# Performance work log

Hardware: AMD Instinct MI355X
Metric: run time of the kernel (lower is better)

The kernel has to match this reference:

```python
import jax, jax.numpy as jnp
import numpy as np

EMBED_DIM = 1024
NUM_HEADS = 16
NUM_KV_HEADS = 4
HEAD_DIM = 64
GQA_RATIO = NUM_HEADS // NUM_KV_HEADS
SCALE = 1.0 / np.sqrt(HEAD_DIM).astype(np.float32)
B, L = 1, 4096
NUM_SEQS = 8  # 8 packed sequences of length 512


def setup_inputs() -> dict:
    key = jax.random.key(0)
    k1, k2, k3, k4, k5 = jax.random.split(key, 5)
    hidden_states = jax.random.normal(k1, (B, L, EMBED_DIM), dtype=jnp.float32)
    cu_seqlens = (jnp.arange(NUM_SEQS + 1, dtype=jnp.int32) * (L // NUM_SEQS))
    s = 1.0 / np.sqrt(EMBED_DIM)
    Wq = jax.random.normal(k2, (EMBED_DIM, NUM_HEADS * HEAD_DIM), dtype=jnp.float32) * s
    Wk = jax.random.normal(k3, (EMBED_DIM, NUM_KV_HEADS * HEAD_DIM), dtype=jnp.float32) * s
    Wv = jax.random.normal(k4, (EMBED_DIM, NUM_KV_HEADS * HEAD_DIM), dtype=jnp.float32) * s
    Wo = jax.random.normal(k5, (NUM_HEADS * HEAD_DIM, EMBED_DIM), dtype=jnp.float32) * s
    return {"hidden_states": hidden_states, "Wq": Wq, "Wk": Wk, "Wv": Wv, "Wo": Wo,
            "cu_seqlens": cu_seqlens}


def reference(hidden_states, Wq, Wk, Wv, Wo, cu_seqlens):
    b, l, d = hidden_states.shape
    # QKV projections (Linear, no bias)
    q = (hidden_states @ Wq).reshape(b, l, NUM_HEADS, HEAD_DIM)
    k = (hidden_states @ Wk).reshape(b, l, NUM_KV_HEADS, HEAD_DIM)
    v = (hidden_states @ Wv).reshape(b, l, NUM_KV_HEADS, HEAD_DIM)
    # GQA: expand kv heads to num_heads (faithful to module's manual expand)
    k = jnp.repeat(k, GQA_RATIO, axis=2)  # [b, l, H, hd]
    v = jnp.repeat(v, GQA_RATIO, axis=2)
    # [b, H, l, hd]
    q = q.transpose(0, 2, 1, 3)
    k = k.transpose(0, 2, 1, 3)
    v = v.transpose(0, 2, 1, 3)
    # block-diagonal varlen mask from cu_seqlens
    pos = jnp.arange(l, dtype=jnp.int32)
    seq_ids = jnp.searchsorted(cu_seqlens, pos, side='right') - 1  # [l]
    mask = seq_ids[:, None] == seq_ids[None, :]                    # [l, l]
    # dense SDPA with mask
    scores = jnp.einsum('bhqd,bhkd->bhqk', q, k) * SCALE
    scores = jnp.where(mask[None, None], scores, jnp.finfo(scores.dtype).min)
    attn = jax.nn.softmax(scores, axis=-1)
    out = jnp.einsum('bhqk,bhkd->bhqd', attn, v)
    out = out.transpose(0, 2, 1, 3).reshape(b, l, NUM_HEADS * HEAD_DIM)
    return out @ Wo
```

## Files before the change

### kernel.cpp

```cpp
#include <hip/hip_runtime.h>
#include <hip/hip_bf16.h>
#include <stdint.h>
#include <stddef.h>

typedef __attribute__((ext_vector_type(8))) short short8;
typedef __attribute__((ext_vector_type(4))) short short4v;
typedef __attribute__((ext_vector_type(4))) float f32x4;

__device__ inline void store_c(float* p, float v) { *p = v; }
__device__ inline void store_c(__hip_bfloat16* p, float v) { *p = __float2bfloat16(v); }

__device__ __forceinline__ void gld_lds16(const __hip_bfloat16* g, __hip_bfloat16* l)
{
#if __has_builtin(__builtin_amdgcn_global_load_lds)
    __builtin_amdgcn_global_load_lds(
        (const __attribute__((address_space(1))) unsigned int*)g,
        (__attribute__((address_space(3))) unsigned int*)l,
        16, 0, 0);
#else
    *(short8*)((char*)l + (threadIdx.x & 63) * 16) = *(const short8*)g;
#endif
}

__global__ __launch_bounds__(256) void convert_kernel(const float* __restrict__ in,
                                                      __hip_bfloat16* __restrict__ out,
                                                      int n4)
{
    int i = blockIdx.x * blockDim.x + threadIdx.x;
    if (i >= n4) return;
    const f32x4 v = *(const f32x4*)(in + (size_t)i * 4);
    union { __hip_bfloat16 t[4]; short4v s4; } u;
    #pragma unroll
    for (int j = 0; j < 4; ++j) u.t[j] = __float2bfloat16(v[j]);
    *(short4v*)(out + (size_t)i * 4) = u.s4;
}

__global__ __launch_bounds__(256) void transpose_kernel(const float* __restrict__ Wq,
                                                        const float* __restrict__ Wk,
                                                        const float* __restrict__ Wv,
                                                        const float* __restrict__ Wo,
                                                        __hip_bfloat16* __restrict__ Wt)
{
    __shared__ float tile[32][33];
    const int bk = blockIdx.x;
    const int bn = blockIdx.y;
    const int tx = threadIdx.x & 31;
    const int ty = threadIdx.x >> 5;
    const int n0 = bn * 32;

    const float* src; int ld; int col0;
    if (n0 < 1024)      { src = Wq; ld = 1024; col0 = n0; }
    else if (n0 < 1280) { src = Wk; ld = 256;  col0 = n0 - 1024; }
    else if (n0 < 1536) { src = Wv; ld = 256;  col0 = n0 - 1280; }
    else                { src = Wo; ld = 1024; col0 = n0 - 1536; }

    #pragma unroll
    for (int r = 0; r < 4; ++r) {
        int k = ty + 8 * r;
        tile[k][tx] = src[(size_t)(bk * 32 + k) * ld + col0 + tx];
    }
    __syncthreads();
    #pragma unroll
    for (int r = 0; r < 4; ++r) {
        int nl = ty + 8 * r;
        Wt[(size_t)(n0 + nl) * 1024 + bk * 32 + tx] = __float2bfloat16(tile[tx][nl]);
    }
}

__global__ __launch_bounds__(256) void vt_kernel(const __hip_bfloat16* __restrict__ QKV,
                                                 __hip_bfloat16* __restrict__ Vt)
{
    __shared__ __hip_bfloat16 tile[32][34];
    const int j0 = blockIdx.x * 32;
    const int c0 = blockIdx.y * 32;
    const int tx = threadIdx.x & 31;
    const int ty = threadIdx.x >> 5;

    #pragma unroll
    for (int r = 0; r < 4; ++r) {
        int jl = ty + 8 * r;
        int j = j0 + jl;
        int srcrow = (j & ~63) + (j & 3) * 16 + ((j >> 2) & 15);
        tile[jl][tx] = QKV[(size_t)srcrow * 1536 + 1280 + c0 + tx];
    }
    __syncthreads();
    #pragma unroll
    for (int r = 0; r < 4; ++r) {
        int cl = ty + 8 * r;
        Vt[(size_t)(c0 + cl) * 4096 + j0 + tx] = tile[tx][cl];
    }
}

#define BK 32

template <int BM, int BN, typename CT>
__global__ __launch_bounds__(256) void gemm_gld_kernel(const __hip_bfloat16* __restrict__ A,
                                                       const __hip_bfloat16* __restrict__ Bt,
                                                       CT* __restrict__ C,
                                                       int M, int N, int K)
{
    constexpr int MF = BM / 32;
    constexpr int NF = BN / 32;
    __shared__ __align__(16) __hip_bfloat16 As[BM * BK];
    __shared__ __align__(16) __hip_bfloat16 Bs[BN * BK];

    const int tid  = threadIdx.x;
    const int lane = tid & 63;
    const int wave = tid >> 6;
    const int wm = wave >> 1;
    const int wn = wave & 1;
    const int fr = lane & 15;
    const int fk = (lane >> 4) * 8;

    const __hip_bfloat16* Ab = A  + (size_t)(blockIdx.x * BM) * K;
    const __hip_bfloat16* Bb = Bt + (size_t)(blockIdx.y * BN) * K;

    const int srow = lane >> 2;
    const int scol = (lane & 3) * 8;

    f32x4 acc[MF][NF];
    const f32x4 z4 = {0.f, 0.f, 0.f, 0.f};
    #pragma unroll
    for (int i = 0; i < MF; ++i)
        #pragma unroll
        for (int j = 0; j < NF; ++j) acc[i][j] = z4;

    for (int k0 = 0; k0 < K; k0 += BK) {
        for (int i = wave; i < BM / 16; i += 4)
            gld_lds16(Ab + (size_t)(i * 16 + srow) * K + k0 + scol, &As[i * 512]);
        for (int i = wave; i < BN / 16; i += 4)
            gld_lds16(Bb + (size_t)(i * 16 + srow) * K + k0 + scol, &Bs[i * 512]);
        __syncthreads();

        short8 af[MF], bfv[NF];
        #pragma unroll
        for (int mf = 0; mf < MF; ++mf)
            af[mf] = *(const short8*)&As[(wm * (BM / 2) + mf * 16 + fr) * BK + fk];
        #pragma unroll
        for (int nf = 0; nf < NF; ++nf)
            bfv[nf] = *(const short8*)&Bs[(wn * (BN / 2) + nf * 16 + fr) * BK + fk];
        #pragma unroll
        for (int mf = 0; mf < MF; ++mf)
            #pragma unroll
            for (int nf = 0; nf < NF; ++nf)
                acc[mf][nf] = __builtin_amdgcn_mfma_f32_16x16x32_bf16(af[mf], bfv[nf], acc[mf][nf], 0, 0, 0);
        __syncthreads();
    }

    const int crow = blockIdx.x * BM + wm * (BM / 2);
    const int ccol = blockIdx.y * BN + wn * (BN / 2);
    #pragma unroll
    for (int mf = 0; mf < MF; ++mf)
        #pragma unroll
        for (int nf = 0; nf < NF; ++nf)
            #pragma unroll
            for (int r = 0; r < 4; ++r) {
                int row = crow + mf * 16 + (lane >> 4) * 4 + r;
                int col = ccol + nf * 16 + fr;
                store_c(&C[(size_t)row * N + col], acc[mf][nf][r]);
            }
}

__global__ __launch_bounds__(256) void attn_kernel(const __hip_bfloat16* __restrict__ QKV,
                                                   const __hip_bfloat16* __restrict__ Vt,
                                                   __hip_bfloat16* __restrict__ O)
{
    __shared__ __align__(16) __hip_bfloat16 Ks[64 * 64];
    __shared__ __align__(16) __hip_bfloat16 Vts[64 * 64];
    __shared__ __align__(16) __hip_bfloat16 Ps[4][16][72];

    const int tid  = threadIdx.x;
    const int lane = tid & 63;
    const int wave = tid >> 6;
    const int qt = blockIdx.x;
    const int h  = blockIdx.y;
    const int sq = blockIdx.z;
    const int kvh = h >> 2;

    const int fr = lane & 15;
    const int fg = lane >> 4;
    const int fk = fg * 8;

    const int sr = lane >> 3;
    const int scol = ((lane & 7) ^ sr) * 8;

    const int q0 = sq * 512 + qt * 64 + wave * 16;

    short8 qf[2];
    #pragma unroll
    for (int kc = 0; kc < 2; ++kc)
        qf[kc] = *(const short8*)(QKV + (size_t)(q0 + fr) * 1536 + h * 64 + kc * 32 + fk);

    const f32x4 z4 = {0.f, 0.f, 0.f, 0.f};
    f32x4 acc_o[4];
    #pragma unroll
    for (int b = 0; b < 4; ++b) acc_o[b] = z4;

    float m_run[4], l_run[4];
    #pragma unroll
    for (int r = 0; r < 4; ++r) { m_run[r] = -1e30f; l_run[r] = 0.f; }

    const float cs = 0.125f * 1.44269504088896340736f;

    for (int t = 0; t < 8; ++t) {
        const int kvbase = sq * 512 + t * 64;

        #pragma unroll
        for (int i = wave; i < 8; i += 4) {
            gld_lds16(QKV + (size_t)(kvbase + i * 8 + sr) * 1536 + 1024 + kvh * 64 + scol,
                      &Ks[i * 512]);
            gld_lds16(Vt + (size_t)(kvh * 64 + i * 8 + sr) * 4096 + kvbase + scol,
                      &Vts[i * 512]);
        }
        __syncthreads();

        f32x4 s[4];
        #pragma unroll
        for (int b = 0; b < 4; ++b) s[b] = z4;
        #pragma unroll
        for (int kc = 0; kc < 2; ++kc) {
            #pragma unroll
            for (int nf = 0; nf < 4; ++nf) {
                short8 kf = *(const short8*)&Ks[(nf * 16 + fr) * 64 + (((kc * 4 + fg) ^ (fr & 7)) * 8)];
                s[nf] = __builtin_amdgcn_mfma_f32_16x16x32_bf16(qf[kc], kf, s[nf], 0, 0, 0);
            }
        }

        #pragma unroll
        for (int r = 0; r < 4; ++r) {
            float mx = fmaxf(fmaxf(s[0][r], s[1][r]), fmaxf(s[2][r], s[3][r]));
            #pragma unroll
            for (int off = 1; off < 16; off <<= 1)
                mx = fmaxf(mx, __shfl_xor(mx, off));
            float mnew = fmaxf(m_run[r], mx);
            float f = exp2f((m_run[r] - mnew) * cs);
            m_run[r] = mnew;
            float p0 = exp2f((s[0][r] - mnew) * cs);
            float p1 = exp2f((s[1][r] - mnew) * cs);
            float p2 = exp2f((s[2][r] - mnew) * cs);
            float p3 = exp2f((s[3][r] - mnew) * cs);
            l_run[r] = l_run[r] * f + (p0 + p1 + p2 + p3);
            #pragma unroll
            for (int nf = 0; nf < 4; ++nf)
                acc_o[nf][r] *= f;
            int rl = fg * 4 + r;
            union { __hip_bfloat16 h[4]; short4v s4; } pw;
            pw.h[0] = __float2bfloat16(p0);
            pw.h[1] = __float2bfloat16(p1);
            pw.h[2] = __float2bfloat16(p2);
            pw.h[3] = __float2bfloat16(p3);
            *(short4v*)&Ps[wave][rl][fr * 4] = pw.s4;
        }

        #pragma unroll
        for (int kc = 0; kc < 2; ++kc) {
            short8 pa = *(const short8*)&Ps[wave][fr][kc * 32 + fk];
            #pragma unroll
            for (int nf = 0; nf < 4; ++nf) {
                short8 vf = *(const short8*)&Vts[(nf * 16 + fr) * 64 + (((kc * 4 + fg) ^ (fr & 7)) * 8)];
                acc_o[nf] = __builtin_amdgcn_mfma_f32_16x16x32_bf16(pa, vf, acc_o[nf], 0, 0, 0);
            }
        }
        __syncthreads();
    }

    #pragma unroll
    for (int r = 0; r < 4; ++r) {
        float lsum = l_run[r];
        #pragma unroll
        for (int off = 1; off < 16; off <<= 1)
            lsum += __shfl_xor(lsum, off);
        float inv_l = 1.0f / lsum;
        int row = q0 + fg * 4 + r;
        #pragma unroll
        for (int nf = 0; nf < 4; ++nf)
            O[(size_t)row * 1024 + h * 64 + nf * 16 + fr] =
                __float2bfloat16(acc_o[nf][r] * inv_l);
    }
}

extern "C" void kernel_launch(void* const* d_in, const int* in_sizes, int n_in,
                              void* d_out, int out_size, void* d_ws, size_t ws_size,
                              hipStream_t stream)
{
    const float* hs = (const float*)d_in[0];
    const float* Wq = (const float*)d_in[1];
    const float* Wk = (const float*)d_in[2];
    const float* Wv = (const float*)d_in[3];
    const float* Wo = (const float*)d_in[4];

    char* ws = (char*)d_ws;
    __hip_bfloat16* hsb  = (__hip_bfloat16*)(ws);
    __hip_bfloat16* Wt   = (__hip_bfloat16*)(ws + 8388608);
    __hip_bfloat16* QKV  = (__hip_bfloat16*)(ws + 13631488);
    __hip_bfloat16* AOut = (__hip_bfloat16*)(ws + 26214400);
    __hip_bfloat16* Vt   = (__hip_bfloat16*)(ws + 34603008);
    float* out = (float*)d_out;

    convert_kernel<<<4096, 256, 0, stream>>>(hs, hsb, 1048576);
    transpose_kernel<<<dim3(32, 80), 256, 0, stream>>>(Wq, Wk, Wv, Wo, Wt);
    gemm_gld_kernel<64, 128, __hip_bfloat16><<<dim3(64, 12), 256, 0, stream>>>(hsb, Wt, QKV, 4096, 1536, 1024);
    vt_kernel<<<dim3(128, 8), 256, 0, stream>>>(QKV, Vt);
    attn_kernel<<<dim3(8, 16, 8), 256, 0, stream>>>(QKV, Vt, AOut);
    gemm_gld_kernel<64, 128, float><<<dim3(64, 8), 256, 0, stream>>>(AOut, Wt + (size_t)1536 * 1024, out, 4096, 1024, 1024);
}
```

Baseline: 158.9 us.

## Use 128x128 GEMM tiles with BK=64, 8 waves and XOR-swizzled LDS

Replaces the 64x128/BK=32 GEMM with a 128x128 tile kernel using 512 threads, a K step of 64, and an XOR swizzle on the LDS layout so fragment reads avoid bank conflicts. Larger tiles raise reuse per loaded byte and halve the number of barrier-separated K iterations. In exchange the grid shrinks to 384 and 256 blocks, which may underfill the 256 CUs and leave little latency hiding, since there is still no double buffering.

```diff
diff --git a/kernel.cpp b/kernel.cpp
--- a/kernel.cpp
+++ b/kernel.cpp
@@ -91,71 +91,82 @@
     }
 }
 
-#define BK 32
-
-template <int BM, int BN, typename CT>
-__global__ __launch_bounds__(256) void gemm_gld_kernel(const __hip_bfloat16* __restrict__ A,
-                                                       const __hip_bfloat16* __restrict__ Bt,
-                                                       CT* __restrict__ C,
-                                                       int M, int N, int K)
-{
-    constexpr int MF = BM / 32;
-    constexpr int NF = BN / 32;
-    __shared__ __align__(16) __hip_bfloat16 As[BM * BK];
-    __shared__ __align__(16) __hip_bfloat16 Bs[BN * BK];
+template <typename CT>
+__global__ __launch_bounds__(512) void gemm128_kernel(const __hip_bfloat16* __restrict__ A,
+                                                      const __hip_bfloat16* __restrict__ Bt,
+                                                      CT* __restrict__ C,
+                                                      int M, int N, int K)
+{
+    __shared__ __align__(16) __hip_bfloat16 As[128 * 64];
+    __shared__ __align__(16) __hip_bfloat16 Bs[128 * 64];
 
     const int tid  = threadIdx.x;
     const int lane = tid & 63;
     const int wave = tid >> 6;
-    const int wm = wave >> 1;
-    const int wn = wave & 1;
+    const int wr = wave >> 2;
+    const int wc = wave & 3;
     const int fr = lane & 15;
-    const int fk = (lane >> 4) * 8;
-
-    const __hip_bfloat16* Ab = A  + (size_t)(blockIdx.x * BM) * K;
-    const __hip_bfloat16* Bb = Bt + (size_t)(blockIdx.y * BN) * K;
-
-    const int srow = lane >> 2;
-    const int scol = (lane & 3) * 8;
-
-    f32x4 acc[MF][NF];
+    const int fg = lane >> 4;
+
+    const __hip_bfloat16* Ab = A  + (size_t)(blockIdx.x * 128) * K;
+    const __hip_bfloat16* Bb = Bt + (size_t)(blockIdx.y * 128) * K;
+
+    const int srow8 = lane >> 3;
+    const int sslot = (lane & 7) ^ srow8;
+
+    f32x4 acc[4][2];
     const f32x4 z4 = {0.f, 0.f, 0.f, 0.f};
     #pragma unroll
-    for (int i = 0; i < MF; ++i)
-        #pragma unroll
-        for (int j = 0; j < NF; ++j) acc[i][j] = z4;
-
-    for (int k0 = 0; k0 < K; k0 += BK) {
-        for (int i = wave; i < BM / 16; i += 4)
-            gld_lds16(Ab + (size_t)(i * 16 + srow) * K + k0 + scol, &As[i * 512]);
-        for (int i = wave; i < BN / 16; i += 4)
-            gld_lds16(Bb + (size_t)(i * 16 + srow) * K + k0 + scol, &Bs[i * 512]);
+    for (int i = 0; i < 4; ++i)
+        #pragma unroll
+        for (int j = 0; j < 2; ++j) acc[i][j] = z4;
+
+    for (int k0 = 0; k0 < K; k0 += 64) {
+        #pragma unroll
+        for (int i = 0; i < 2; ++i) {
+            int c = wave * 2 + i;
+            gld_lds16(Ab + (size_t)(c * 8 + srow8) * K + k0 + sslot * 8, &As[c * 512]);
+        }
+        #pragma unroll
+        for (int i = 0; i < 2; ++i) {
+            int c = wave * 2 + i;
+            gld_lds16(Bb + (size_t)(c * 8 + srow8) * K + k0 + sslot * 8, &Bs[c * 512]);
+        }
         __syncthreads();
 
-        short8 af[MF], bfv[NF];
-        #pragma unroll
-        for (int mf = 0; mf < MF; ++mf)
-            af[mf] = *(const short8*)&As[(wm * (BM / 2) + mf * 16 + fr) * BK + fk];
-        #pragma unroll
-        for (int nf = 0; nf < NF; ++nf)
-            bfv[nf] = *(const short8*)&Bs[(wn * (BN / 2) + nf * 16 + fr) * BK + fk];
-        #pragma unroll
-        for (int mf = 0; mf < MF; ++mf)
-            #pragma unroll
-            for (int nf = 0; nf < NF; ++nf)
-                acc[mf][nf] = __builtin_amdgcn_mfma_f32_16x16x32_bf16(af[mf], bfv[nf], acc[mf][nf], 0, 0, 0);
+        short8 af[2][4], bfv[2][2];
+        #pragma unroll
+        for (int kc = 0; kc < 2; ++kc) {
+            #pragma unroll
+            for (int mf = 0; mf < 4; ++mf) {
+                int rr = wr * 64 + mf * 16 + fr;
+                af[kc][mf] = *(const short8*)&As[rr * 64 + (((kc * 4 + fg) ^ (fr & 7)) * 8)];
+            }
+            #pragma unroll
+            for (int nf = 0; nf < 2; ++nf) {
+                int cc = wc * 32 + nf * 16 + fr;
+                bfv[kc][nf] = *(const short8*)&Bs[cc * 64 + (((kc * 4 + fg) ^ (fr & 7)) * 8)];
+            }
+        }
+        #pragma unroll
+        for (int kc = 0; kc < 2; ++kc)
+            #pragma unroll
+            for (int mf = 0; mf < 4; ++mf)
+                #pragma unroll
+                for (int nf = 0; nf < 2; ++nf)
+                    acc[mf][nf] = __builtin_amdgcn_mfma_f32_16x16x32_bf16(af[kc][mf], bfv[kc][nf], acc[mf][nf], 0, 0, 0);
         __syncthreads();
     }
 
-    const int crow = blockIdx.x * BM + wm * (BM / 2);
-    const int ccol = blockIdx.y * BN + wn * (BN / 2);
-    #pragma unroll
-    for (int mf = 0; mf < MF; ++mf)
-        #pragma unroll
-        for (int nf = 0; nf < NF; ++nf)
+    const int crow = blockIdx.x * 128 + wr * 64;
+    const int ccol = blockIdx.y * 128 + wc * 32;
+    #pragma unroll
+    for (int mf = 0; mf < 4; ++mf)
+        #pragma unroll
+        for (int nf = 0; nf < 2; ++nf)
             #pragma unroll
             for (int r = 0; r < 4; ++r) {
-                int row = crow + mf * 16 + (lane >> 4) * 4 + r;
+                int row = crow + mf * 16 + fg * 4 + r;
                 int col = ccol + nf * 16 + fr;
                 store_c(&C[(size_t)row * N + col], acc[mf][nf][r]);
             }
@@ -299,8 +310,8 @@
 
     convert_kernel<<<4096, 256, 0, stream>>>(hs, hsb, 1048576);
     transpose_kernel<<<dim3(32, 80), 256, 0, stream>>>(Wq, Wk, Wv, Wo, Wt);
-    gemm_gld_kernel<64, 128, __hip_bfloat16><<<dim3(64, 12), 256, 0, stream>>>(hsb, Wt, QKV, 4096, 1536, 1024);
+    gemm128_kernel<__hip_bfloat16><<<dim3(32, 12), 512, 0, stream>>>(hsb, Wt, QKV, 4096, 1536, 1024);
     vt_kernel<<<dim3(128, 8), 256, 0, stream>>>(QKV, Vt);
     attn_kernel<<<dim3(8, 16, 8), 256, 0, stream>>>(QKV, Vt, AOut);
-    gemm_gld_kernel<64, 128, float><<<dim3(64, 8), 256, 0, stream>>>(AOut, Wt + (size_t)1536 * 1024, out, 4096, 1024, 1024);
-}
+    gemm128_kernel<float><<<dim3(32, 8), 512, 0, stream>>>(AOut, Wt + (size_t)1536 * 1024, out, 4096, 1024, 1024);
+}
```

Result: faster. 154.3 us (-2.9%).
